# Optimization experiments

Measured on AMD Instinct MI355X. Metric: run time of the kernel, lower is better.

Reference implementation:

```python
import jax, jax.numpy as jnp
import numpy as np

Q = 200000       # number of logical qubits
C = 64           # number of cores
D = 128          # core_emb_shape == d_E == d_H


def setup_inputs() -> dict:
    key = jax.random.key(0)
    k1, k2, k3, k4, k5, k6 = jax.random.split(key, 6)
    prev_assign = jax.random.randint(k1, (Q,), 0, C)
    q_embeddings = jax.random.normal(k2, (Q, D), dtype=jnp.float32)
    padding_emb = jnp.zeros((D,), dtype=jnp.float32)
    # symmetric 0/1 core connectivity matrix
    a = (jax.random.uniform(k3, (C, C)) < 0.3).astype(jnp.float32)
    core_con = jnp.maximum(a, a.T) * (1.0 - jnp.eye(C, dtype=jnp.float32))
    # single GNN layer params: relu(X Wself + A X Wmsg + b)
    W_self = jax.random.normal(k4, (D, D), dtype=jnp.float32) / np.sqrt(D)
    W_msg = jax.random.normal(k5, (D, D), dtype=jnp.float32) / np.sqrt(D)
    b = jax.random.normal(k6, (D,), dtype=jnp.float32) * 0.01
    return {"prev_assign": prev_assign, "q_embeddings": q_embeddings,
            "padding_emb": padding_emb, "core_con": core_con,
            "W_self": W_self, "W_msg": W_msg, "b": b}


def reference(prev_assign, q_embeddings, padding_emb, core_con, W_self, W_msg, b):
    n_cores = core_con.shape[0]
    # fused per-core max-reduce over qubit embeddings grouped by prev_assign
    seg_max = jax.ops.segment_max(q_embeddings, prev_assign, num_segments=n_cores)  # [C, D]
    counts = jax.ops.segment_sum(jnp.ones((q_embeddings.shape[0],), q_embeddings.dtype),
                                 prev_assign, num_segments=n_cores)                 # [C]
    core_embs = jnp.where((counts > 0)[:, None], seg_max, padding_emb[None, :])     # [C, D]
    # GNN over core connectivity graph (single message-passing layer)
    msg = core_con @ (core_embs @ W_msg)            # [C, D]
    return jax.nn.relu(core_embs @ W_self + msg + b)  # [C, D]
```

## Files before the change

### kernel.cpp

```cpp
#include <hip/hip_runtime.h>
#include <math.h>

#define D 128
#define C 64
#define P1_THREADS 256
#define P1_GRID 512

__device__ __forceinline__ unsigned f2key(float f) {
  unsigned u = __float_as_uint(f);
  return (u & 0x80000000u) ? ~u : (u | 0x80000000u);
}
__device__ __forceinline__ float key2f(unsigned k) {
  unsigned u = (k & 0x80000000u) ? (k & 0x7fffffffu) : ~k;
  return __uint_as_float(u);
}

__global__ __launch_bounds__(P1_THREADS) void p1_segmax(
    const int* __restrict__ assign, const float* __restrict__ qe,
    unsigned* __restrict__ part, int Q, int niter) {
  __shared__ unsigned buf[C * D];
  int tid = threadIdx.x;
  for (int i = tid; i < C * D; i += P1_THREADS) buf[i] = 0u;
  __syncthreads();

  int lane = tid & 31;
  int r = tid >> 5;

  for (int it = blockIdx.x; it < niter; it += gridDim.x) {
    int base = it * 32;
    if (base + 32 <= Q) {
      float4 v[4];
      int a[4];
#pragma unroll
      for (int i = 0; i < 4; ++i) {
        int row = base + i * 8 + r;
        v[i] = *(const float4*)&qe[(size_t)row * D + lane * 4];
        a[i] = assign[row] * D + lane;
      }
#pragma unroll
      for (int i = 0; i < 4; ++i) {
        atomicMax(&buf[a[i] +  0], f2key(v[i].x));
        atomicMax(&buf[a[i] + 32], f2key(v[i].y));
        atomicMax(&buf[a[i] + 64], f2key(v[i].z));
        atomicMax(&buf[a[i] + 96], f2key(v[i].w));
      }
    } else {
      for (int i = 0; i < 4; ++i) {
        int row = base + i * 8 + r;
        if (row < Q) {
          float4 v = *(const float4*)&qe[(size_t)row * D + lane * 4];
          int a = assign[row] * D + lane;
          atomicMax(&buf[a +  0], f2key(v.x));
          atomicMax(&buf[a + 32], f2key(v.y));
          atomicMax(&buf[a + 64], f2key(v.z));
          atomicMax(&buf[a + 96], f2key(v.w));
        }
      }
    }
  }
  __syncthreads();

  unsigned* outp = part + (size_t)blockIdx.x * (C * D);
  for (int i = tid; i < C * D; i += P1_THREADS) {
    int d = i & 127;
    outp[i] = buf[(i & ~127) + (d & 3) * 32 + (d >> 2)];
  }
}

__global__ __launch_bounds__(256) void p2_merge(
    const unsigned* __restrict__ part, const float* __restrict__ padding,
    float* __restrict__ core_embs, int nb) {
  __shared__ unsigned red[256];
  int tid = threadIdx.x;
  int o_local = tid & 63;
  int rdr = tid >> 6;
  int o = blockIdx.x * 64 + o_local;
  unsigned m = 0u;
#pragma unroll 8
  for (int br = rdr; br < nb; br += 4)
    m = max(m, part[(size_t)br * (C * D) + o]);
  red[tid] = m;
  __syncthreads();
  if (tid < 64) {
    unsigned k = max(max(red[tid], red[tid + 64]),
                     max(red[tid + 128], red[tid + 192]));
    core_embs[o] = k ? key2f(k) : padding[o & (D - 1)];
  }
}

__global__ __launch_bounds__(D) void p3a_gemm(
    const float* __restrict__ core_embs, const float* __restrict__ Wmsg,
    float* __restrict__ tmp) {
  __shared__ float xrow[D];
  int t = threadIdx.x;
  int j = blockIdx.x;
  xrow[t] = core_embs[j * D + t];
  __syncthreads();
  float acc = 0.f;
#pragma unroll 8
  for (int k = 0; k < D; ++k) acc += xrow[k] * Wmsg[k * D + t];
  tmp[j * D + t] = acc;
}

__global__ __launch_bounds__(D) void p3b_out(
    const float* __restrict__ core_embs, const float* __restrict__ con,
    const float* __restrict__ tmp, const float* __restrict__ Wself,
    const float* __restrict__ b, float* __restrict__ out) {
  __shared__ float ce[D];
  __shared__ float cr[C];
  int t = threadIdx.x;
  int c = blockIdx.x;
  ce[t] = core_embs[c * D + t];
  if (t < C) cr[t] = con[c * C + t];
  __syncthreads();
  float acc = b[t];
#pragma unroll 8
  for (int k = 0; k < D; ++k) acc += ce[k] * Wself[k * D + t];
#pragma unroll 8
  for (int j = 0; j < C; ++j) acc += cr[j] * tmp[j * D + t];
  out[c * D + t] = fmaxf(acc, 0.f);
}

extern "C" void kernel_launch(void* const* d_in, const int* in_sizes, int n_in,
                              void* d_out, int out_size, void* d_ws, size_t ws_size,
                              hipStream_t stream) {
  const int* assign    = (const int*)d_in[0];
  const float* qe      = (const float*)d_in[1];
  const float* padding = (const float*)d_in[2];
  const float* con     = (const float*)d_in[3];
  const float* Wself   = (const float*)d_in[4];
  const float* Wmsg    = (const float*)d_in[5];
  const float* b       = (const float*)d_in[6];
  float* out = (float*)d_out;
  int Q = in_sizes[0];

  const size_t slot = (size_t)C * D;
  size_t avail = ws_size / 4;
  long nb_max = (long)((avail > 2 * slot ? avail - 2 * slot : slot) / slot);
  int nb = (int)(nb_max < P1_GRID ? nb_max : P1_GRID);
  if (nb < 1) nb = 1;

  unsigned* part   = (unsigned*)d_ws;
  float* core_embs = (float*)((unsigned*)d_ws + (size_t)nb * slot);
  float* tmp       = core_embs + slot;

  int niter = (Q + 31) / 32;

  hipLaunchKernelGGL(p1_segmax, dim3(nb), dim3(P1_THREADS), 0, stream,
                     assign, qe, part, Q, niter);
  hipLaunchKernelGGL(p2_merge, dim3((C * D) / 64), dim3(256), 0, stream,
                     part, padding, core_embs, nb);
  hipLaunchKernelGGL(p3a_gemm, dim3(C), dim3(D), 0, stream,
                     core_embs, Wmsg, tmp);
  hipLaunchKernelGGL(p3b_out, dim3(C), dim3(D), 0, stream,
                     core_embs, con, tmp, Wself, b, out);
}
```

Baseline: 187.2 us.

## Merge block partials with global atomicMax and fuse GNN stages into one kernel

Per-block shared-memory max results are merged straight into one global key array with atomicMax, which removes the partial-buffer writes and the separate merge kernel. A small init kernel zeroes the key array first. The two GEMM kernels become one fused kernel that decodes the keys, computes con·CE, and then applies Wself and Wmsg, reordering the maths to (A X) Wmsg. In exchange, every block redundantly decodes all keys and recomputes A·X for its row, and global atomic contention rises across 512 blocks.

```diff
diff --git a/kernel.cpp b/kernel.cpp
--- a/kernel.cpp
+++ b/kernel.cpp
@@ -15,9 +15,13 @@
   return __uint_as_float(u);
 }
 
+__global__ __launch_bounds__(256) void p0_init(unsigned* __restrict__ keys) {
+  keys[blockIdx.x * 256 + threadIdx.x] = 0u;
+}
+
 __global__ __launch_bounds__(P1_THREADS) void p1_segmax(
     const int* __restrict__ assign, const float* __restrict__ qe,
-    unsigned* __restrict__ part, int Q, int niter) {
+    unsigned* __restrict__ gkeys, int Q, int niter) {
   __shared__ unsigned buf[C * D];
   int tid = threadIdx.x;
   for (int i = tid; i < C * D; i += P1_THREADS) buf[i] = 0u;
@@ -60,64 +64,39 @@
   }
   __syncthreads();
 
-  unsigned* outp = part + (size_t)blockIdx.x * (C * D);
   for (int i = tid; i < C * D; i += P1_THREADS) {
     int d = i & 127;
-    outp[i] = buf[(i & ~127) + (d & 3) * 32 + (d >> 2)];
+    unsigned v = buf[(i & ~127) + (d & 3) * 32 + (d >> 2)];
+    if (v) atomicMax(&gkeys[i], v);
   }
 }
 
-__global__ __launch_bounds__(256) void p2_merge(
-    const unsigned* __restrict__ part, const float* __restrict__ padding,
-    float* __restrict__ core_embs, int nb) {
-  __shared__ unsigned red[256];
-  int tid = threadIdx.x;
-  int o_local = tid & 63;
-  int rdr = tid >> 6;
-  int o = blockIdx.x * 64 + o_local;
-  unsigned m = 0u;
-#pragma unroll 8
-  for (int br = rdr; br < nb; br += 4)
-    m = max(m, part[(size_t)br * (C * D) + o]);
-  red[tid] = m;
-  __syncthreads();
-  if (tid < 64) {
-    unsigned k = max(max(red[tid], red[tid + 64]),
-                     max(red[tid + 128], red[tid + 192]));
-    core_embs[o] = k ? key2f(k) : padding[o & (D - 1)];
-  }
-}
-
-__global__ __launch_bounds__(D) void p3a_gemm(
-    const float* __restrict__ core_embs, const float* __restrict__ Wmsg,
-    float* __restrict__ tmp) {
-  __shared__ float xrow[D];
-  int t = threadIdx.x;
-  int j = blockIdx.x;
-  xrow[t] = core_embs[j * D + t];
-  __syncthreads();
-  float acc = 0.f;
-#pragma unroll 8
-  for (int k = 0; k < D; ++k) acc += xrow[k] * Wmsg[k * D + t];
-  tmp[j * D + t] = acc;
-}
-
-__global__ __launch_bounds__(D) void p3b_out(
-    const float* __restrict__ core_embs, const float* __restrict__ con,
-    const float* __restrict__ tmp, const float* __restrict__ Wself,
-    const float* __restrict__ b, float* __restrict__ out) {
-  __shared__ float ce[D];
-  __shared__ float cr[C];
+__global__ __launch_bounds__(D) void p3_fused(
+    const unsigned* __restrict__ keys, const float* __restrict__ padding,
+    const float* __restrict__ con, const float* __restrict__ Wself,
+    const float* __restrict__ Wmsg, const float* __restrict__ b,
+    float* __restrict__ out) {
+  __shared__ float CE[C * D];
+  __shared__ float Mrow[D];
+  __shared__ float crow[C];
   int t = threadIdx.x;
   int c = blockIdx.x;
-  ce[t] = core_embs[c * D + t];
-  if (t < C) cr[t] = con[c * C + t];
+  for (int i = t; i < C * D; i += D) {
+    unsigned k = keys[i];
+    CE[i] = k ? key2f(k) : padding[i & (D - 1)];
+  }
+  if (t < C) crow[t] = con[c * C + t];
+  __syncthreads();
+  float m = 0.f;
+#pragma unroll 8
+  for (int j = 0; j < C; ++j) m += crow[j] * CE[j * D + t];
+  Mrow[t] = m;
   __syncthreads();
   float acc = b[t];
 #pragma unroll 8
-  for (int k = 0; k < D; ++k) acc += ce[k] * Wself[k * D + t];
+  for (int k = 0; k < D; ++k) acc += CE[c * D + k] * Wself[k * D + t];
 #pragma unroll 8
-  for (int j = 0; j < C; ++j) acc += cr[j] * tmp[j * D + t];
+  for (int k = 0; k < D; ++k) acc += Mrow[k] * Wmsg[k * D + t];
   out[c * D + t] = fmaxf(acc, 0.f);
 }
 
@@ -134,24 +113,12 @@
   float* out = (float*)d_out;
   int Q = in_sizes[0];
 
-  const size_t slot = (size_t)C * D;
-  size_t avail = ws_size / 4;
-  long nb_max = (long)((avail > 2 * slot ? avail - 2 * slot : slot) / slot);
-  int nb = (int)(nb_max < P1_GRID ? nb_max : P1_GRID);
-  if (nb < 1) nb = 1;
-
-  unsigned* part   = (unsigned*)d_ws;
-  float* core_embs = (float*)((unsigned*)d_ws + (size_t)nb * slot);
-  float* tmp       = core_embs + slot;
-
+  unsigned* gkeys = (unsigned*)d_ws;
   int niter = (Q + 31) / 32;
 
-  hipLaunchKernelGGL(p1_segmax, dim3(nb), dim3(P1_THREADS), 0, stream,
-                     assign, qe, part, Q, niter);
-  hipLaunchKernelGGL(p2_merge, dim3((C * D) / 64), dim3(256), 0, stream,
-                     part, padding, core_embs, nb);
-  hipLaunchKernelGGL(p3a_gemm, dim3(C), dim3(D), 0, stream,
-                     core_embs, Wmsg, tmp);
-  hipLaunchKernelGGL(p3b_out, dim3(C), dim3(D), 0, stream,
-                     core_embs, con, tmp, Wself, b, out);
+  hipLaunchKernelGGL(p0_init, dim3((C * D) / 256), dim3(256), 0, stream, gkeys);
+  hipLaunchKernelGGL(p1_segmax, dim3(P1_GRID), dim3(P1_THREADS), 0, stream,
+                     assign, qe, gkeys, Q, niter);
+  hipLaunchKernelGGL(p3_fused, dim3(C), dim3(D), 0, stream,
+                     gkeys, padding, con, Wself, Wmsg, b, out);
 }
```

Result: slower. 205.8 us (+9.9%).

## Fuse GNN GEMMs into one kernel by reassociating con@(X@Wmsg)

Applied to the files above, without the earlier changes.

Replaces the two tail kernels with a single kernel. Each block loads the whole core-embedding matrix into shared memory, computes its row of core_con @ X first, then multiplies that row by W_msg and adds X@W_self, so the intermediate buffer and one launch go away. The price is redundant work: every block reloads the 32 KB embedding matrix into shared memory, and the larger shared footprint may limit occupancy.

```diff
diff --git a/kernel.cpp b/kernel.cpp
--- a/kernel.cpp
+++ b/kernel.cpp
@@ -88,36 +88,28 @@
   }
 }
 
-__global__ __launch_bounds__(D) void p3a_gemm(
-    const float* __restrict__ core_embs, const float* __restrict__ Wmsg,
-    float* __restrict__ tmp) {
-  __shared__ float xrow[D];
-  int t = threadIdx.x;
-  int j = blockIdx.x;
-  xrow[t] = core_embs[j * D + t];
-  __syncthreads();
-  float acc = 0.f;
-#pragma unroll 8
-  for (int k = 0; k < D; ++k) acc += xrow[k] * Wmsg[k * D + t];
-  tmp[j * D + t] = acc;
-}
-
-__global__ __launch_bounds__(D) void p3b_out(
+__global__ __launch_bounds__(D) void p3_fused(
     const float* __restrict__ core_embs, const float* __restrict__ con,
-    const float* __restrict__ tmp, const float* __restrict__ Wself,
+    const float* __restrict__ Wself, const float* __restrict__ Wmsg,
     const float* __restrict__ b, float* __restrict__ out) {
-  __shared__ float ce[D];
-  __shared__ float cr[C];
+  __shared__ float CE[C * D];
+  __shared__ float Mrow[D];
+  __shared__ float crow[C];
   int t = threadIdx.x;
   int c = blockIdx.x;
-  ce[t] = core_embs[c * D + t];
-  if (t < C) cr[t] = con[c * C + t];
+  for (int i = t; i < C * D; i += D) CE[i] = core_embs[i];
+  if (t < C) crow[t] = con[c * C + t];
+  __syncthreads();
+  float m = 0.f;
+#pragma unroll 8
+  for (int j = 0; j < C; ++j) m += crow[j] * CE[j * D + t];
+  Mrow[t] = m;
   __syncthreads();
   float acc = b[t];
 #pragma unroll 8
-  for (int k = 0; k < D; ++k) acc += ce[k] * Wself[k * D + t];
+  for (int k = 0; k < D; ++k) acc += CE[c * D + k] * Wself[k * D + t];
 #pragma unroll 8
-  for (int j = 0; j < C; ++j) acc += cr[j] * tmp[j * D + t];
+  for (int k = 0; k < D; ++k) acc += Mrow[k] * Wmsg[k * D + t];
   out[c * D + t] = fmaxf(acc, 0.f);
 }
 
@@ -136,13 +128,12 @@
 
   const size_t slot = (size_t)C * D;
   size_t avail = ws_size / 4;
-  long nb_max = (long)((avail > 2 * slot ? avail - 2 * slot : slot) / slot);
+  long nb_max = (long)((avail > slot ? avail - slot : slot) / slot);
   int nb = (int)(nb_max < P1_GRID ? nb_max : P1_GRID);
   if (nb < 1) nb = 1;
 
   unsigned* part   = (unsigned*)d_ws;
   float* core_embs = (float*)((unsigned*)d_ws + (size_t)nb * slot);
-  float* tmp       = core_embs + slot;
 
   int niter = (Q + 31) / 32;
 
@@ -150,8 +141,6 @@
                      assign, qe, part, Q, niter);
   hipLaunchKernelGGL(p2_merge, dim3((C * D) / 64), dim3(256), 0, stream,
                      part, padding, core_embs, nb);
-  hipLaunchKernelGGL(p3a_gemm, dim3(C), dim3(D), 0, stream,
-                     core_embs, Wmsg, tmp);
-  hipLaunchKernelGGL(p3b_out, dim3(C), dim3(D), 0, stream,
-                     core_embs, con, tmp, Wself, b, out);
+  hipLaunchKernelGGL(p3_fused, dim3(C), dim3(D), 0, stream,
+                     core_embs, con, Wself, Wmsg, b, out);
 }
```

New measurement: 186.5 us. Within noise of the previous version (-0.4%).
